# Performance work log

Measured on AMD Instinct MI355X. Metric: run time of the kernel, lower is better.

## Reference

```python
import jax, jax.numpy as jnp
import numpy as np

N_NODES = 100000
N_EDGES = 1600000
NFEAT, NHID, NCLASS = 128, 64, 16


def gcn_conv(x, W, edge_index, edge_weight, num_nodes):
    # PyG GCNConv (normalize=False, add_self_loops=False, bias=False):
    # h = x @ W ; out[i] = sum over edges (j->i) of edge_weight * h[j]
    h = x @ W                                  # [N, out]
    src, dst = edge_index[0], edge_index[1]
    msgs = h[src] * edge_weight[:, None]       # [E, out] gathered messages
    return jax.ops.segment_sum(msgs, dst, num_segments=num_nodes)


def setup_inputs() -> dict:
    key = jax.random.key(0)
    k = jax.random.split(key, 7)
    x = jax.random.normal(k[0], (N_NODES, NFEAT), dtype=jnp.float32)
    edge_index1 = jax.random.randint(k[1], (2, N_EDGES), 0, N_NODES, dtype=jnp.int32)
    edge_index2 = jax.random.randint(k[2], (2, N_EDGES), 0, N_NODES, dtype=jnp.int32)
    edge_weight1 = jax.random.uniform(k[3], (N_EDGES,), dtype=jnp.float32)
    edge_weight2 = jax.random.uniform(k[4], (N_EDGES,), dtype=jnp.float32)
    # Glorot-style linear weights (GCNConv lin, bias=False)
    W1 = jax.random.normal(k[5], (NFEAT, NHID), dtype=jnp.float32) / np.sqrt(NFEAT)
    W2 = jax.random.normal(k[6], (NHID, NCLASS), dtype=jnp.float32) / np.sqrt(NHID)
    return {"x": x, "edge_index1": edge_index1, "edge_index2": edge_index2,
            "edge_weight1": edge_weight1, "edge_weight2": edge_weight2,
            "W1": W1, "W2": W2}


def reference(x, edge_index1, edge_index2, edge_weight1, edge_weight2, W1, W2):
    n = x.shape[0]
    h = jax.nn.relu(gcn_conv(x, W1, edge_index1, edge_weight1, n))
    out = gcn_conv(h, W2, edge_index2, edge_weight2, n)
    return out
```

## Files before the change

kernel.cpp:

```cpp
#include <hip/hip_runtime.h>
#include <hip/hip_bf16.h>


#define EPB 4096
#define NBMAX 512
#define CAP 6144


__global__ __launch_bounds__(128) void gemm1_kernel(const float* __restrict__ x,
                                                    const float* __restrict__ W1,
                                                    __hip_bfloat16* __restrict__ h1,
                                                    int n_nodes) {
    __shared__ float As[32][132];
    __shared__ float Bs[32][64];
    int tid = threadIdx.x;
    int node0 = blockIdx.x * 128;
    int n8 = (tid & 15) * 8;
    int f8 = (tid >> 4) * 8;
    float acc[8][8];
#pragma unroll
    for (int i = 0; i < 8; ++i)
#pragma unroll
        for (int j = 0; j < 8; ++j) acc[i][j] = 0.f;

    const float4* x4 = reinterpret_cast<const float4*>(x);
    const float4* W4 = reinterpret_cast<const float4*>(W1);

    for (int s = 0; s < 4; ++s) {
#pragma unroll
        for (int j = 0; j < 8; ++j) {
            int idx = tid + j * 128;
            int n = idx >> 3;
            int kq = idx & 7;
            float4 v = make_float4(0.f, 0.f, 0.f, 0.f);
            if (node0 + n < n_nodes) v = x4[(size_t)(node0 + n) * 32 + s * 8 + kq];
            int k4 = kq * 4;
            As[k4 + 0][n] = v.x;
            As[k4 + 1][n] = v.y;
            As[k4 + 2][n] = v.z;
            As[k4 + 3][n] = v.w;
        }
#pragma unroll
        for (int j = 0; j < 4; ++j) {
            int idx = tid + j * 128;
            int k = idx >> 4;
            int fq = idx & 15;
            *reinterpret_cast<float4*>(&Bs[k][fq * 4]) = W4[(size_t)(s * 32 + k) * 16 + fq];
        }
        __syncthreads();
#pragma unroll
        for (int kk = 0; kk < 32; ++kk) {
            float4 a0 = *reinterpret_cast<const float4*>(&As[kk][n8]);
            float4 a1 = *reinterpret_cast<const float4*>(&As[kk][n8 + 4]);
            float4 b0 = *reinterpret_cast<const float4*>(&Bs[kk][f8]);
            float4 b1 = *reinterpret_cast<const float4*>(&Bs[kk][f8 + 4]);
            float av[8] = {a0.x, a0.y, a0.z, a0.w, a1.x, a1.y, a1.z, a1.w};
            float bv[8] = {b0.x, b0.y, b0.z, b0.w, b1.x, b1.y, b1.z, b1.w};
#pragma unroll
            for (int i = 0; i < 8; ++i)
#pragma unroll
                for (int j = 0; j < 8; ++j) acc[i][j] += av[i] * bv[j];
        }
        __syncthreads();
    }
#pragma unroll
    for (int i = 0; i < 8; ++i) {
        int n = node0 + n8 + i;
        if (n < n_nodes) {
            __hip_bfloat16 tmp[8];
#pragma unroll
            for (int j = 0; j < 8; ++j) tmp[j] = __float2bfloat16(acc[i][j]);
            *reinterpret_cast<uint4*>(&h1[(size_t)n * 64 + f8]) =
                *reinterpret_cast<const uint4*>(tmp);
        }
    }
}


__global__ void bin_hist_kernel(const int* __restrict__ ei1, const int* __restrict__ ei2,
                                int* __restrict__ hist_g, int n_edges, int nblk, int nb) {
    __shared__ int hist[NBMAX];
    int tid = threadIdx.x, blk = blockIdx.x;
    int layer = (blk >= nblk) ? 1 : 0;
    int lblk = blk - layer * nblk;
    const int* ei = layer ? ei2 : ei1;
    for (int i = tid; i < nb; i += 256) hist[i] = 0;
    __syncthreads();
    int e0 = lblk * EPB;
#pragma unroll
    for (int j = 0; j < EPB / 256; ++j) {
        int e = e0 + tid + j * 256;
        if (e < n_edges) atomicAdd(&hist[ei[n_edges + e] >> 8], 1);
    }
    __syncthreads();
    int base = layer * nb * nblk;
    for (int i = tid; i < nb; i += 256) hist_g[base + i * nblk + lblk] = hist[i];
}

__global__ void scan_local_k(int* __restrict__ data, int* __restrict__ bsums, int n) {
    __shared__ int tmp[1024];
    int i = blockIdx.x * 1024 + threadIdx.x;
    int v = (i < n) ? data[i] : 0;
    tmp[threadIdx.x] = v;
    __syncthreads();
    for (int off = 1; off < 1024; off <<= 1) {
        int t = (threadIdx.x >= off) ? tmp[threadIdx.x - off] : 0;
        __syncthreads();
        tmp[threadIdx.x] += t;
        __syncthreads();
    }
    if (i < n) data[i] = tmp[threadIdx.x] - v;
    if (threadIdx.x == 1023) bsums[blockIdx.x] = tmp[1023];
}

__global__ void scan_top_k(int* __restrict__ bsums, int nbk) {
    __shared__ int tmp[512];
    int v = (threadIdx.x < nbk) ? bsums[threadIdx.x] : 0;
    tmp[threadIdx.x] = v;
    __syncthreads();
    for (int off = 1; off < 512; off <<= 1) {
        int t = (threadIdx.x >= off) ? tmp[threadIdx.x - off] : 0;
        __syncthreads();
        tmp[threadIdx.x] += t;
        __syncthreads();
    }
    if (threadIdx.x < nbk) bsums[threadIdx.x] = tmp[threadIdx.x] - v;
}

__global__ void add_offsets_k(int* __restrict__ data, const int* __restrict__ bsums, int n) {
    int i = blockIdx.x * 1024 + threadIdx.x;
    if (i < n) data[i] += bsums[blockIdx.x];
}

__global__ void bin_scatter_kernel(const int* __restrict__ ei1, const int* __restrict__ ei2,
                                   const float* __restrict__ ew1, const float* __restrict__ ew2,
                                   const int* __restrict__ scan_g, int2* __restrict__ rec_out,
                                   int n_edges, int nblk, int nb) {
    __shared__ int2 srec[EPB];
    __shared__ unsigned short sbkt[EPB];
    __shared__ int loff[NBMAX], cur[NBMAX], gbase[NBMAX];
    __shared__ int p[256];
    int tid = threadIdx.x, blk = blockIdx.x;
    int layer = (blk >= nblk) ? 1 : 0;
    int lblk = blk - layer * nblk;
    const int* ei = layer ? ei2 : ei1;
    const float* ew = layer ? ew2 : ew1;
    int n_scan_tot = 2 * nb * nblk;
    int total = 2 * n_edges;
    int base = layer * nb * nblk;
    int e0 = lblk * EPB;
    int cnt = min(EPB, n_edges - e0);
    for (int i = tid; i < nb; i += 256) {
        int l = base + i * nblk + lblk;
        int g = scan_g[l];
        int nxt = (l + 1 < n_scan_tot) ? scan_g[l + 1] : total;
        gbase[i] = g;
        loff[i] = nxt - g;
    }
    __syncthreads();
    int b0 = tid * 2;
    int c0 = (b0 < nb) ? loff[b0] : 0;
    int c1 = (b0 + 1 < nb) ? loff[b0 + 1] : 0;
    p[tid] = c0 + c1;
    __syncthreads();
    for (int off = 1; off < 256; off <<= 1) {
        int t = (tid >= off) ? p[tid - off] : 0;
        __syncthreads();
        p[tid] += t;
        __syncthreads();
    }
    int pbase = (tid > 0) ? p[tid - 1] : 0;
    __syncthreads();
    if (b0 < nb)     { loff[b0] = pbase;          cur[b0] = pbase; }
    if (b0 + 1 < nb) { loff[b0 + 1] = pbase + c0; cur[b0 + 1] = pbase + c0; }
    __syncthreads();
#pragma unroll
    for (int j = 0; j < EPB / 256; ++j) {
        int e = e0 + tid + j * 256;
        if (e < n_edges) {
            int s = ei[e], d = ei[n_edges + e];
            int b = d >> 8;
            int r = atomicAdd(&cur[b], 1);
            srec[r] = make_int2(s | ((d & 255) << 20), __float_as_int(ew[e]));
            sbkt[r] = (unsigned short)b;
        }
    }
    __syncthreads();
    for (int i = tid; i < cnt; i += 256) {
        int b = sbkt[i];
        rec_out[gbase[b] + (i - loff[b])] = srec[i];
    }
}


__global__ __launch_bounds__(256) void bucket_sort_kernel(
        const int2* __restrict__ rec_in, const int* __restrict__ scan_g,
        int2* __restrict__ rec_out, int* __restrict__ rowptr1, int* __restrict__ rowptr2,
        int n_nodes, int n_edges, int nblk, int nb) {
    __shared__ int2 srec[CAP];
    __shared__ int hist[256], cur[256], rp[256];
    int tid = threadIdx.x, b = blockIdx.x;
    int layer = (b >= nb) ? 1 : 0;
    int lb = b - layer * nb;
    int* rowptr = layer ? rowptr2 : rowptr1;
    int total = 2 * n_edges;
    int start = scan_g[b * nblk];
    int end = (b + 1 < 2 * nb) ? scan_g[(b + 1) * nblk] : total;
    int cnt = end - start;
    hist[tid] = 0;
    __syncthreads();
    for (int i = tid; i < cnt; i += 256) {
        int2 r = rec_in[start + i];
        atomicAdd(&hist[(r.x >> 20) & 255], 1);
    }
    __syncthreads();
    int v = hist[tid];
    rp[tid] = v;
    __syncthreads();
    for (int off = 1; off < 256; off <<= 1) {
        int t = (tid >= off) ? rp[tid - off] : 0;
        __syncthreads();
        rp[tid] += t;
        __syncthreads();
    }
    int excl = rp[tid] - v;
    cur[tid] = excl;
    int node = (lb << 8) + tid;
    if (node < n_nodes) rowptr[node] = start + excl;
    if (lb == nb - 1 && tid == 0) rowptr[n_nodes] = end;
    __syncthreads();
    for (int i = tid; i < cnt; i += 256) {
        int2 r = rec_in[start + i];
        int rk = atomicAdd(&cur[(r.x >> 20) & 255], 1);
        if (rk < CAP) srec[rk] = r;
    }
    __syncthreads();
    int lim = min(cnt, CAP);
    for (int i = tid; i < lim; i += 256) rec_out[start + i] = srec[i];
}


__global__ __launch_bounds__(256) void gather1_kernel(const __hip_bfloat16* __restrict__ h1,
                                                      const int* __restrict__ rowptr,
                                                      const int2* __restrict__ rec,
                                                      const float* __restrict__ W2,
                                                      float* __restrict__ h2, int n_nodes) {
    int tid = threadIdx.x;
    int w = tid >> 6, f = tid & 63;
    int n = blockIdx.x * 4 + w;
    bool valid = (n < n_nodes);
    int i = 0, end = 0;
    if (valid) { i = rowptr[n]; end = rowptr[n + 1]; }
    float a0 = 0.f, a1 = 0.f, a2 = 0.f, a3 = 0.f;
    float a4 = 0.f, a5 = 0.f, a6 = 0.f, a7 = 0.f;
    for (; i + 7 < end; i += 8) {
        int2 r0 = rec[i],     r1 = rec[i + 1], r2 = rec[i + 2], r3 = rec[i + 3];
        int2 r4 = rec[i + 4], r5 = rec[i + 5], r6 = rec[i + 6], r7 = rec[i + 7];
        a0 += __bfloat162float(h1[(size_t)(r0.x & 0xFFFFF) * 64 + f]) * __int_as_float(r0.y);
        a1 += __bfloat162float(h1[(size_t)(r1.x & 0xFFFFF) * 64 + f]) * __int_as_float(r1.y);
        a2 += __bfloat162float(h1[(size_t)(r2.x & 0xFFFFF) * 64 + f]) * __int_as_float(r2.y);
        a3 += __bfloat162float(h1[(size_t)(r3.x & 0xFFFFF) * 64 + f]) * __int_as_float(r3.y);
        a4 += __bfloat162float(h1[(size_t)(r4.x & 0xFFFFF) * 64 + f]) * __int_as_float(r4.y);
        a5 += __bfloat162float(h1[(size_t)(r5.x & 0xFFFFF) * 64 + f]) * __int_as_float(r5.y);
        a6 += __bfloat162float(h1[(size_t)(r6.x & 0xFFFFF) * 64 + f]) * __int_as_float(r6.y);
        a7 += __bfloat162float(h1[(size_t)(r7.x & 0xFFFFF) * 64 + f]) * __int_as_float(r7.y);
    }
    for (; i + 3 < end; i += 4) {
        int2 r0 = rec[i], r1 = rec[i + 1], r2 = rec[i + 2], r3 = rec[i + 3];
        a0 += __bfloat162float(h1[(size_t)(r0.x & 0xFFFFF) * 64 + f]) * __int_as_float(r0.y);
        a1 += __bfloat162float(h1[(size_t)(r1.x & 0xFFFFF) * 64 + f]) * __int_as_float(r1.y);
        a2 += __bfloat162float(h1[(size_t)(r2.x & 0xFFFFF) * 64 + f]) * __int_as_float(r2.y);
        a3 += __bfloat162float(h1[(size_t)(r3.x & 0xFFFFF) * 64 + f]) * __int_as_float(r3.y);
    }
    for (; i < end; ++i) {
        int2 r = rec[i];
        a0 += __bfloat162float(h1[(size_t)(r.x & 0xFFFFF) * 64 + f]) * __int_as_float(r.y);
    }
    float r = fmaxf(((a0 + a1) + (a2 + a3)) + ((a4 + a5) + (a6 + a7)), 0.f);
    int c = f & 15, kq = f >> 4;
    float pacc = 0.f;
#pragma unroll
    for (int j = 0; j < 16; ++j) {
        int k = kq * 16 + j;
        float rk = __shfl(r, k, 64);
        pacc += rk * W2[k * 16 + c];
    }
    pacc += __shfl_xor(pacc, 16, 64);
    pacc += __shfl_xor(pacc, 32, 64);
    if (valid && f < 16) h2[(size_t)n * 16 + f] = pacc;
}


__global__ void gather2_kernel(const float* __restrict__ h2,
                               const int* __restrict__ rowptr,
                               const int2* __restrict__ rec,
                               float* __restrict__ out, int n_nodes) {
    int n = blockIdx.x * 16 + (threadIdx.x >> 4);
    if (n >= n_nodes) return;
    int f = threadIdx.x & 15;
    int i = rowptr[n], end = rowptr[n + 1];
    float a0 = 0.f, a1 = 0.f, a2 = 0.f, a3 = 0.f;
    float a4 = 0.f, a5 = 0.f, a6 = 0.f, a7 = 0.f;
    for (; i + 7 < end; i += 8) {
        int2 r0 = rec[i],     r1 = rec[i + 1], r2 = rec[i + 2], r3 = rec[i + 3];
        int2 r4 = rec[i + 4], r5 = rec[i + 5], r6 = rec[i + 6], r7 = rec[i + 7];
        a0 += h2[(size_t)(r0.x & 0xFFFFF) * 16 + f] * __int_as_float(r0.y);
        a1 += h2[(size_t)(r1.x & 0xFFFFF) * 16 + f] * __int_as_float(r1.y);
        a2 += h2[(size_t)(r2.x & 0xFFFFF) * 16 + f] * __int_as_float(r2.y);
        a3 += h2[(size_t)(r3.x & 0xFFFFF) * 16 + f] * __int_as_float(r3.y);
        a4 += h2[(size_t)(r4.x & 0xFFFFF) * 16 + f] * __int_as_float(r4.y);
        a5 += h2[(size_t)(r5.x & 0xFFFFF) * 16 + f] * __int_as_float(r5.y);
        a6 += h2[(size_t)(r6.x & 0xFFFFF) * 16 + f] * __int_as_float(r6.y);
        a7 += h2[(size_t)(r7.x & 0xFFFFF) * 16 + f] * __int_as_float(r7.y);
    }
    for (; i + 3 < end; i += 4) {
        int2 r0 = rec[i], r1 = rec[i + 1], r2 = rec[i + 2], r3 = rec[i + 3];
        a0 += h2[(size_t)(r0.x & 0xFFFFF) * 16 + f] * __int_as_float(r0.y);
        a1 += h2[(size_t)(r1.x & 0xFFFFF) * 16 + f] * __int_as_float(r1.y);
        a2 += h2[(size_t)(r2.x & 0xFFFFF) * 16 + f] * __int_as_float(r2.y);
        a3 += h2[(size_t)(r3.x & 0xFFFFF) * 16 + f] * __int_as_float(r3.y);
    }
    for (; i < end; ++i) {
        int2 r = rec[i];
        a0 += h2[(size_t)(r.x & 0xFFFFF) * 16 + f] * __int_as_float(r.y);
    }
    out[(size_t)n * 16 + f] = (((a0 + a1) + (a2 + a3)) + ((a4 + a5) + (a6 + a7)));
}


extern "C" void kernel_launch(void* const* d_in, const int* in_sizes, int n_in,
                              void* d_out, int out_size, void* d_ws, size_t ws_size,
                              hipStream_t stream) {
    const float* x   = (const float*)d_in[0];
    const int*   ei1 = (const int*)d_in[1];
    const int*   ei2 = (const int*)d_in[2];
    const float* ew1 = (const float*)d_in[3];
    const float* ew2 = (const float*)d_in[4];
    const float* W1  = (const float*)d_in[5];
    const float* W2  = (const float*)d_in[6];

    const int n_nodes = in_sizes[0] / 128;
    const int n_edges = in_sizes[1] / 2;
    const int nb   = (n_nodes + 255) >> 8;
    const int nblk = (n_edges + EPB - 1) / EPB;
    const int n_scan_tot = 2 * nb * nblk;
    const int scan_blocks = (n_scan_tot + 1023) / 1024;

    int2* rec2   = (int2*)d_ws;
    int2* recbuf = rec2 + (size_t)2 * n_edges;
    int*  hist_g = (int*)(recbuf + (size_t)2 * n_edges);
    int*  bsums  = hist_g + n_scan_tot;
    int*  rowptr1 = bsums + 512;
    int*  rowptr2 = rowptr1 + n_nodes + 1;
    __hip_bfloat16* h1 = (__hip_bfloat16*)recbuf;
    float* h2 = (float*)recbuf + (size_t)n_nodes * 32;
    float* out = (float*)d_out;

    bin_hist_kernel<<<2 * nblk, 256, 0, stream>>>(ei1, ei2, hist_g, n_edges, nblk, nb);
    scan_local_k<<<scan_blocks, 1024, 0, stream>>>(hist_g, bsums, n_scan_tot);
    scan_top_k<<<1, 512, 0, stream>>>(bsums, scan_blocks);
    add_offsets_k<<<scan_blocks, 1024, 0, stream>>>(hist_g, bsums, n_scan_tot);
    bin_scatter_kernel<<<2 * nblk, 256, 0, stream>>>(ei1, ei2, ew1, ew2, hist_g, recbuf,
                                                     n_edges, nblk, nb);
    bucket_sort_kernel<<<2 * nb, 256, 0, stream>>>(recbuf, hist_g, rec2, rowptr1, rowptr2,
                                                   n_nodes, n_edges, nblk, nb);

    gemm1_kernel<<<(n_nodes + 127) / 128, 128, 0, stream>>>(x, W1, h1, n_nodes);
    gather1_kernel<<<(n_nodes + 3) / 4, 256, 0, stream>>>(h1, rowptr1, rec2, W2, h2, n_nodes);
    gather2_kernel<<<(n_nodes + 15) / 16, 256, 0, stream>>>(h2, rowptr2, rec2, out, n_nodes);
}
```

Before: 336.0 us.

## Fuse GEMM1 with edge histogram kernel and unroll gather1 to 16 edges

Merges the x@W1 GEMM into the binning histogram launch by giving the combined grid separate GEMM blocks and histogram blocks. The GEMM now runs before the sort, overlapped with independent work. h1 moves out of the scatter buffer into its own workspace region so the later scatter does not overwrite it. The GEMM block is retiled to 256 threads with a 4x8 per-thread tile, and the gather1 inner loop is unrolled to 16 independent accumulators to expose more memory-level parallelism. This costs extra workspace and higher register pressure in gather1.

Measured after the change: 305.2 us. 9.2% less time.

```diff
diff --git a/kernel.cpp b/kernel.cpp
--- a/kernel.cpp
+++ b/kernel.cpp
@@ -6,95 +6,94 @@
 #define NBMAX 512
 #define CAP 6144
 
-
-__global__ __launch_bounds__(128) void gemm1_kernel(const float* __restrict__ x,
-                                                    const float* __restrict__ W1,
-                                                    __hip_bfloat16* __restrict__ h1,
-                                                    int n_nodes) {
+__global__ __launch_bounds__(256) void gemm1_hist_kernel(
+        const float* __restrict__ x, const float* __restrict__ W1,
+        __hip_bfloat16* __restrict__ h1,
+        const int* __restrict__ ei1, const int* __restrict__ ei2,
+        int* __restrict__ hist_g, int n_nodes, int n_edges, int nblk, int nb,
+        int gemm_blocks) {
     __shared__ float As[32][132];
     __shared__ float Bs[32][64];
+    __shared__ int hist[NBMAX];
     int tid = threadIdx.x;
-    int node0 = blockIdx.x * 128;
-    int n8 = (tid & 15) * 8;
-    int f8 = (tid >> 4) * 8;
-    float acc[8][8];
-#pragma unroll
-    for (int i = 0; i < 8; ++i)
-#pragma unroll
-        for (int j = 0; j < 8; ++j) acc[i][j] = 0.f;
-
-    const float4* x4 = reinterpret_cast<const float4*>(x);
-    const float4* W4 = reinterpret_cast<const float4*>(W1);
-
-    for (int s = 0; s < 4; ++s) {
-#pragma unroll
-        for (int j = 0; j < 8; ++j) {
-            int idx = tid + j * 128;
-            int n = idx >> 3;
-            int kq = idx & 7;
-            float4 v = make_float4(0.f, 0.f, 0.f, 0.f);
-            if (node0 + n < n_nodes) v = x4[(size_t)(node0 + n) * 32 + s * 8 + kq];
-            int k4 = kq * 4;
-            As[k4 + 0][n] = v.x;
-            As[k4 + 1][n] = v.y;
-            As[k4 + 2][n] = v.z;
-            As[k4 + 3][n] = v.w;
+
+    if (blockIdx.x < gemm_blocks) {
+        int node0 = blockIdx.x * 128;
+        int n4 = (tid & 31) * 4;
+        int f8 = (tid >> 5) * 8;
+        float acc[4][8];
+#pragma unroll
+        for (int i = 0; i < 4; ++i)
+#pragma unroll
+            for (int j = 0; j < 8; ++j) acc[i][j] = 0.f;
+
+        const float4* x4 = reinterpret_cast<const float4*>(x);
+        const float4* W4 = reinterpret_cast<const float4*>(W1);
+
+        for (int s = 0; s < 4; ++s) {
+#pragma unroll
+            for (int j = 0; j < 4; ++j) {
+                int idx = tid + j * 256;
+                int n = idx >> 3;
+                int kq = idx & 7;
+                float4 v = make_float4(0.f, 0.f, 0.f, 0.f);
+                if (node0 + n < n_nodes) v = x4[(size_t)(node0 + n) * 32 + s * 8 + kq];
+                int k4 = kq * 4;
+                As[k4 + 0][n] = v.x;
+                As[k4 + 1][n] = v.y;
+                As[k4 + 2][n] = v.z;
+                As[k4 + 3][n] = v.w;
+            }
+#pragma unroll
+            for (int j = 0; j < 2; ++j) {
+                int idx = tid + j * 256;
+                int k = idx >> 4;
+                int fq = idx & 15;
+                *reinterpret_cast<float4*>(&Bs[k][fq * 4]) = W4[(size_t)(s * 32 + k) * 16 + fq];
+            }
+            __syncthreads();
+#pragma unroll
+            for (int kk = 0; kk < 32; ++kk) {
+                float4 a = *reinterpret_cast<const float4*>(&As[kk][n4]);
+                float4 b0 = *reinterpret_cast<const float4*>(&Bs[kk][f8]);
+                float4 b1 = *reinterpret_cast<const float4*>(&Bs[kk][f8 + 4]);
+                float av[4] = {a.x, a.y, a.z, a.w};
+                float bv[8] = {b0.x, b0.y, b0.z, b0.w, b1.x, b1.y, b1.z, b1.w};
+#pragma unroll
+                for (int i = 0; i < 4; ++i)
+#pragma unroll
+                    for (int j = 0; j < 8; ++j) acc[i][j] += av[i] * bv[j];
+            }
+            __syncthreads();
         }
 #pragma unroll
-        for (int j = 0; j < 4; ++j) {
-            int idx = tid + j * 128;
-            int k = idx >> 4;
-            int fq = idx & 15;
-            *reinterpret_cast<float4*>(&Bs[k][fq * 4]) = W4[(size_t)(s * 32 + k) * 16 + fq];
+        for (int i = 0; i < 4; ++i) {
+            int n = node0 + n4 + i;
+            if (n < n_nodes) {
+                __hip_bfloat16 tmp[8];
+#pragma unroll
+                for (int j = 0; j < 8; ++j) tmp[j] = __float2bfloat16(acc[i][j]);
+                *reinterpret_cast<uint4*>(&h1[(size_t)n * 64 + f8]) =
+                    *reinterpret_cast<const uint4*>(tmp);
+            }
         }
-        __syncthreads();
-#pragma unroll
-        for (int kk = 0; kk < 32; ++kk) {
-            float4 a0 = *reinterpret_cast<const float4*>(&As[kk][n8]);
-            float4 a1 = *reinterpret_cast<const float4*>(&As[kk][n8 + 4]);
-            float4 b0 = *reinterpret_cast<const float4*>(&Bs[kk][f8]);
-            float4 b1 = *reinterpret_cast<const float4*>(&Bs[kk][f8 + 4]);
-            float av[8] = {a0.x, a0.y, a0.z, a0.w, a1.x, a1.y, a1.z, a1.w};
-            float bv[8] = {b0.x, b0.y, b0.z, b0.w, b1.x, b1.y, b1.z, b1.w};
-#pragma unroll
-            for (int i = 0; i < 8; ++i)
-#pragma unroll
-                for (int j = 0; j < 8; ++j) acc[i][j] += av[i] * bv[j];
+    } else {
+        int blk = blockIdx.x - gemm_blocks;
+        int layer = (blk >= nblk) ? 1 : 0;
+        int lblk = blk - layer * nblk;
+        const int* ei = layer ? ei2 : ei1;
+        for (int i = tid; i < nb; i += 256) hist[i] = 0;
+        __syncthreads();
+        int e0 = lblk * EPB;
+#pragma unroll
+        for (int j = 0; j < EPB / 256; ++j) {
+            int e = e0 + tid + j * 256;
+            if (e < n_edges) atomicAdd(&hist[ei[n_edges + e] >> 8], 1);
         }
         __syncthreads();
-    }
-#pragma unroll
-    for (int i = 0; i < 8; ++i) {
-        int n = node0 + n8 + i;
-        if (n < n_nodes) {
-            __hip_bfloat16 tmp[8];
-#pragma unroll
-            for (int j = 0; j < 8; ++j) tmp[j] = __float2bfloat16(acc[i][j]);
-            *reinterpret_cast<uint4*>(&h1[(size_t)n * 64 + f8]) =
-                *reinterpret_cast<const uint4*>(tmp);
-        }
-    }
-}
-
-
-__global__ void bin_hist_kernel(const int* __restrict__ ei1, const int* __restrict__ ei2,
-                                int* __restrict__ hist_g, int n_edges, int nblk, int nb) {
-    __shared__ int hist[NBMAX];
-    int tid = threadIdx.x, blk = blockIdx.x;
-    int layer = (blk >= nblk) ? 1 : 0;
-    int lblk = blk - layer * nblk;
-    const int* ei = layer ? ei2 : ei1;
-    for (int i = tid; i < nb; i += 256) hist[i] = 0;
-    __syncthreads();
-    int e0 = lblk * EPB;
-#pragma unroll
-    for (int j = 0; j < EPB / 256; ++j) {
-        int e = e0 + tid + j * 256;
-        if (e < n_edges) atomicAdd(&hist[ei[n_edges + e] >> 8], 1);
-    }
-    __syncthreads();
-    int base = layer * nb * nblk;
-    for (int i = tid; i < nb; i += 256) hist_g[base + i * nblk + lblk] = hist[i];
+        int base = layer * nb * nblk;
+        for (int i = tid; i < nb; i += 256) hist_g[base + i * nblk + lblk] = hist[i];
+    }
 }
 
 __global__ void scan_local_k(int* __restrict__ data, int* __restrict__ bsums, int n) {
@@ -240,6 +239,9 @@
 }
 
 
+#define G1_EDGE(rr, aa) \
+    aa += __bfloat162float(h1[(size_t)((rr).x & 0xFFFFF) * 64 + f]) * __int_as_float((rr).y)
+
 __global__ __launch_bounds__(256) void gather1_kernel(const __hip_bfloat16* __restrict__ h1,
                                                       const int* __restrict__ rowptr,
                                                       const int2* __restrict__ rec,
@@ -253,30 +255,35 @@
     if (valid) { i = rowptr[n]; end = rowptr[n + 1]; }
     float a0 = 0.f, a1 = 0.f, a2 = 0.f, a3 = 0.f;
     float a4 = 0.f, a5 = 0.f, a6 = 0.f, a7 = 0.f;
+    float a8 = 0.f, a9 = 0.f, a10 = 0.f, a11 = 0.f;
+    float a12 = 0.f, a13 = 0.f, a14 = 0.f, a15 = 0.f;
+    for (; i + 15 < end; i += 16) {
+        int2 r0 = rec[i],      r1 = rec[i + 1],  r2 = rec[i + 2],  r3 = rec[i + 3];
+        int2 r4 = rec[i + 4],  r5 = rec[i + 5],  r6 = rec[i + 6],  r7 = rec[i + 7];
+        int2 r8 = rec[i + 8],  r9 = rec[i + 9],  r10 = rec[i + 10], r11 = rec[i + 11];
+        int2 r12 = rec[i + 12], r13 = rec[i + 13], r14 = rec[i + 14], r15 = rec[i + 15];
+        G1_EDGE(r0, a0);   G1_EDGE(r1, a1);   G1_EDGE(r2, a2);   G1_EDGE(r3, a3);
+        G1_EDGE(r4, a4);   G1_EDGE(r5, a5);   G1_EDGE(r6, a6);   G1_EDGE(r7, a7);
+        G1_EDGE(r8, a8);   G1_EDGE(r9, a9);   G1_EDGE(r10, a10); G1_EDGE(r11, a11);
+        G1_EDGE(r12, a12); G1_EDGE(r13, a13); G1_EDGE(r14, a14); G1_EDGE(r15, a15);
+    }
     for (; i + 7 < end; i += 8) {
         int2 r0 = rec[i],     r1 = rec[i + 1], r2 = rec[i + 2], r3 = rec[i + 3];
         int2 r4 = rec[i + 4], r5 = rec[i + 5], r6 = rec[i + 6], r7 = rec[i + 7];
-        a0 += __bfloat162float(h1[(size_t)(r0.x & 0xFFFFF) * 64 + f]) * __int_as_float(r0.y);
-        a1 += __bfloat162float(h1[(size_t)(r1.x & 0xFFFFF) * 64 + f]) * __int_as_float(r1.y);
-        a2 += __bfloat162float(h1[(size_t)(r2.x & 0xFFFFF) * 64 + f]) * __int_as_float(r2.y);
-        a3 += __bfloat162float(h1[(size_t)(r3.x & 0xFFFFF) * 64 + f]) * __int_as_float(r3.y);
-        a4 += __bfloat162float(h1[(size_t)(r4.x & 0xFFFFF) * 64 + f]) * __int_as_float(r4.y);
-        a5 += __bfloat162float(h1[(size_t)(r5.x & 0xFFFFF) * 64 + f]) * __int_as_float(r5.y);
-        a6 += __bfloat162float(h1[(size_t)(r6.x & 0xFFFFF) * 64 + f]) * __int_as_float(r6.y);
-        a7 += __bfloat162float(h1[(size_t)(r7.x & 0xFFFFF) * 64 + f]) * __int_as_float(r7.y);
+        G1_EDGE(r0, a0); G1_EDGE(r1, a1); G1_EDGE(r2, a2); G1_EDGE(r3, a3);
+        G1_EDGE(r4, a4); G1_EDGE(r5, a5); G1_EDGE(r6, a6); G1_EDGE(r7, a7);
     }
     for (; i + 3 < end; i += 4) {
         int2 r0 = rec[i], r1 = rec[i + 1], r2 = rec[i + 2], r3 = rec[i + 3];
-        a0 += __bfloat162float(h1[(size_t)(r0.x & 0xFFFFF) * 64 + f]) * __int_as_float(r0.y);
-        a1 += __bfloat162float(h1[(size_t)(r1.x & 0xFFFFF) * 64 + f]) * __int_as_float(r1.y);
-        a2 += __bfloat162float(h1[(size_t)(r2.x & 0xFFFFF) * 64 + f]) * __int_as_float(r2.y);
-        a3 += __bfloat162float(h1[(size_t)(r3.x & 0xFFFFF) * 64 + f]) * __int_as_float(r3.y);
+        G1_EDGE(r0, a0); G1_EDGE(r1, a1); G1_EDGE(r2, a2); G1_EDGE(r3, a3);
     }
     for (; i < end; ++i) {
         int2 r = rec[i];
-        a0 += __bfloat162float(h1[(size_t)(r.x & 0xFFFFF) * 64 + f]) * __int_as_float(r.y);
-    }
-    float r = fmaxf(((a0 + a1) + (a2 + a3)) + ((a4 + a5) + (a6 + a7)), 0.f);
+        G1_EDGE(r, a0);
+    }
+    float s0 = ((a0 + a1) + (a2 + a3)) + ((a4 + a5) + (a6 + a7));
+    float s1 = ((a8 + a9) + (a10 + a11)) + ((a12 + a13) + (a14 + a15));
+    float r = fmaxf(s0 + s1, 0.f);
     int c = f & 15, kq = f >> 4;
     float pacc = 0.f;
 #pragma unroll
@@ -345,6 +352,7 @@
     const int nblk = (n_edges + EPB - 1) / EPB;
     const int n_scan_tot = 2 * nb * nblk;
     const int scan_blocks = (n_scan_tot + 1023) / 1024;
+    const int gemm_blocks = (n_nodes + 127) / 128;
 
     int2* rec2   = (int2*)d_ws;
     int2* recbuf = rec2 + (size_t)2 * n_edges;
@@ -352,11 +360,12 @@
     int*  bsums  = hist_g + n_scan_tot;
     int*  rowptr1 = bsums + 512;
     int*  rowptr2 = rowptr1 + n_nodes + 1;
-    __hip_bfloat16* h1 = (__hip_bfloat16*)recbuf;
-    float* h2 = (float*)recbuf + (size_t)n_nodes * 32;
+    __hip_bfloat16* h1 = (__hip_bfloat16*)(rowptr2 + n_nodes + 1);
+    float* h2 = (float*)recbuf;
     float* out = (float*)d_out;
 
-    bin_hist_kernel<<<2 * nblk, 256, 0, stream>>>(ei1, ei2, hist_g, n_edges, nblk, nb);
+    gemm1_hist_kernel<<<gemm_blocks + 2 * nblk, 256, 0, stream>>>(
+        x, W1, h1, ei1, ei2, hist_g, n_nodes, n_edges, nblk, nb, gemm_blocks);
     scan_local_k<<<scan_blocks, 1024, 0, stream>>>(hist_g, bsums, n_scan_tot);
     scan_top_k<<<1, 512, 0, stream>>>(bsums, scan_blocks);
     add_offsets_k<<<scan_blocks, 1024, 0, stream>>>(hist_g, bsums, n_scan_tot);
@@ -365,7 +374,6 @@
     bucket_sort_kernel<<<2 * nb, 256, 0, stream>>>(recbuf, hist_g, rec2, rowptr1, rowptr2,
                                                    n_nodes, n_edges, nblk, nb);
 
-    gemm1_kernel<<<(n_nodes + 127) / 128, 128, 0, stream>>>(x, W1, h1, n_nodes);
     gather1_kernel<<<(n_nodes + 3) / 4, 256, 0, stream>>>(h1, rowptr1, rec2, W2, h2, n_nodes);
     gather2_kernel<<<(n_nodes + 15) / 16, 256, 0, stream>>>(h2, rowptr2, rec2, out, n_nodes);
 }
```
